# Optimization experiments

Hardware: AMD Instinct MI355X
Metric: run time of the kernel (lower is better)

The kernel has to match this reference:

```python
import jax, jax.numpy as jnp
import numpy as np

D_MODEL, DFF, OUT, SEQ = 256, 1024, 32, 512
SIGMA = 0.1          # sigma for q/k/v/z SMC noise
SIGMA_OBS = 0.5      # observation noise


def _layernorm(x, g, b, eps=1e-6):
    mu = jnp.mean(x, axis=-1, keepdims=True)
    var = jnp.mean(jnp.square(x - mu), axis=-1, keepdims=True)
    return (x - mu) * jax.lax.rsqrt(var + eps) * g + b


def _resample(params, i_t, t):
    # params: (B,P,S,D); i_t: (B,P) ancestor indices; resample only the past [:t+1]
    past = jnp.take_along_axis(params[:, :, :t + 1, :], i_t[:, :, None, None], axis=1)
    return jnp.concatenate([past, params[:, :, t + 1:, :]], axis=2)


def setup_inputs() -> dict:
    key = jax.random.key(0)
    ks = jax.random.split(key, 24)
    B, P = 32, 10
    d = {
        'x': jax.random.normal(ks[0], (B, P, D_MODEL), jnp.float32),
        'y': jax.random.normal(ks[1], (B, P, OUT), jnp.float32),
        'K': jax.random.normal(ks[2], (B, P, SEQ, D_MODEL), jnp.float32),
        'V': jax.random.normal(ks[3], (B, P, SEQ, D_MODEL), jnp.float32),
        'R': jax.random.normal(ks[4], (B, P, SEQ, D_MODEL), jnp.float32),
        'noise_q': jax.random.normal(ks[5], (B, P, 1, D_MODEL), jnp.float32),
        'noise_k': jax.random.normal(ks[6], (B, P, 1, D_MODEL), jnp.float32),
        'noise_v': jax.random.normal(ks[7], (B, P, 1, D_MODEL), jnp.float32),
        'noise_z': jax.random.normal(ks[8], (B, P, 1, D_MODEL), jnp.float32),
        'dec_timestep': 256,
    }
    s = 0.02
    d['wq_w'] = jax.random.normal(ks[9], (D_MODEL, D_MODEL), jnp.float32) * s
    d['wq_b'] = jnp.zeros((D_MODEL,), jnp.float32)
    d['wk_w'] = jax.random.normal(ks[10], (D_MODEL, D_MODEL), jnp.float32) * s
    d['wk_b'] = jnp.zeros((D_MODEL,), jnp.float32)
    d['wv_w'] = jax.random.normal(ks[11], (D_MODEL, D_MODEL), jnp.float32) * s
    d['wv_b'] = jnp.zeros((D_MODEL,), jnp.float32)
    d['wz_w'] = jax.random.normal(ks[12], (D_MODEL, D_MODEL), jnp.float32) * s
    d['wz_b'] = jnp.zeros((D_MODEL,), jnp.float32)
    d['ln1_g'] = jnp.ones((D_MODEL,), jnp.float32)
    d['ln1_b'] = jnp.zeros((D_MODEL,), jnp.float32)
    d['ffn_w1'] = jax.random.normal(ks[13], (D_MODEL, DFF), jnp.float32) * s
    d['ffn_b1'] = jnp.zeros((DFF,), jnp.float32)
    d['ffn_w2'] = jax.random.normal(ks[14], (DFF, D_MODEL), jnp.float32) * s
    d['ffn_b2'] = jnp.zeros((D_MODEL,), jnp.float32)
    d['ln2_g'] = jnp.ones((D_MODEL,), jnp.float32)
    d['ln2_b'] = jnp.zeros((D_MODEL,), jnp.float32)
    d['out_w'] = jax.random.normal(ks[15], (D_MODEL, OUT), jnp.float32) * s
    d['out_b'] = jnp.zeros((OUT,), jnp.float32)
    return d


def reference(x, y, K, V, R, noise_q, noise_k, noise_v, noise_z,
              wq_w, wq_b, wk_w, wk_b, wv_w, wv_b, wz_w, wz_b,
              ln1_g, ln1_b, ffn_w1, ffn_b1, ffn_w2, ffn_b2,
              ln2_g, ln2_b, out_w, out_b, dec_timestep):
    t = dec_timestep
    B, P, D = x.shape
    sq = jnp.sqrt(jnp.float32(SIGMA))
    xq = x[:, :, None, :]           # (B,P,1,D)
    yq = y[:, :, None, :]           # (B,P,1,F_y)
    # --- Self_Attention_SMC: project current token, add SMC gaussian noise ---
    q = xq @ wq_w + wq_b + sq * noise_q
    k = xq @ wk_w + wk_b + sq * noise_k
    v = xq @ wv_w + wv_b + sq * noise_v
    # in-place style KV cache update at timestep t (concat past/new/future)
    K = jnp.concatenate([K[:, :, :t, :], k, K[:, :, t + 1:, :]], axis=2)
    V = jnp.concatenate([V[:, :, :t, :], v, V[:, :, t + 1:, :]], axis=2)
    logits = jnp.einsum('bpod,bpsd->bpos', q, K) / jnp.sqrt(jnp.float32(D))
    attn_weights = jax.nn.softmax(logits, axis=-1)          # (B,P,1,S)
    z = jnp.einsum('bpos,bpsd->bpod', attn_weights, V)
    z = z @ wz_w + wz_b + sq * noise_z
    # --- full_model: layernorm + FFN + layernorm ---
    out = _layernorm(z + xq, ln1_g, ln1_b)
    r = jax.nn.relu(out @ ffn_w1 + ffn_b1) @ ffn_w2 + ffn_b2
    r = _layernorm(r + out, ln2_g, ln2_b)                   # (B,P,1,D)
    predictions = r @ out_w + out_b                          # (B,P,1,F_y)
    R = jnp.concatenate([R[:, :, :t, :], r, R[:, :, t + 1:, :]], axis=2)
    mu = jnp.squeeze(yq - predictions, axis=-2)              # (B,P,F_y)
    log_w = -jnp.sum(mu * mu, axis=-1) / (2.0 * SIGMA_OBS)   # (B,P)
    w = jax.nn.softmax(jnp.exp(log_w), axis=-1)              # faithful to original (softmax of exp)
    w = jax.lax.stop_gradient(w)
    # categorical resampling of ancestors (tf.random.categorical uses w as logits)
    i_t = jax.random.categorical(jax.random.key(42), w[:, None, :], shape=(B, P))
    i_t = jax.lax.stop_gradient(i_t)
    K = _resample(K, i_t, t)
    V = _resample(V, i_t, t)
    R = _resample(R, i_t, t)
    return r, attn_weights, K, V, R, w
```

## Files before the change

kernel.cpp:

```cpp
#include <hip/hip_runtime.h>
#include <hip/hip_bf16.h>
#include <stdint.h>

#define BATCH 32
#define NPART 10
#define BP_TOT 320
#define DM 256
#define FF 1024
#define OD 32
#define SL 512
#define NCHUNK 4
#define CROWS 128

#define SQRT_SIGMA 0.31622776601683794f

typedef float nfloat4 __attribute__((ext_vector_type(4)));

__device__ __forceinline__ void nt_store4(const float4& v, float* p) {
    nfloat4 nv;
    nv.x = v.x; nv.y = v.y; nv.z = v.z; nv.w = v.w;
    __builtin_nontemporal_store(nv, (nfloat4*)p);
}

__device__ __forceinline__ uint32_t rotl32(uint32_t x, uint32_t r) {
    return (x << r) | (x >> (32u - r));
}

__device__ __forceinline__ void threefry2x32(uint32_t k0, uint32_t k1,
                                             uint32_t x0, uint32_t x1,
                                             uint32_t& o0, uint32_t& o1) {
    uint32_t k2 = k0 ^ k1 ^ 0x1BD11BDAu;
    uint32_t x = x0 + k0, y = x1 + k1;
#define TFR(r) { x += y; y = rotl32(y, r); y ^= x; }
    TFR(13u) TFR(15u) TFR(26u) TFR(6u)
    x += k1; y += k2 + 1u;
    TFR(17u) TFR(29u) TFR(16u) TFR(24u)
    x += k2; y += k0 + 2u;
    TFR(13u) TFR(15u) TFR(26u) TFR(6u)
    x += k0; y += k1 + 3u;
    TFR(17u) TFR(29u) TFR(16u) TFR(24u)
    x += k1; y += k2 + 4u;
    TFR(13u) TFR(15u) TFR(26u) TFR(6u)
    x += k2; y += k0 + 5u;
#undef TFR
    o0 = x; o1 = y;
}

__device__ __forceinline__ float jax_gumbel_part(uint32_t m) {
    const float TINY = 1.17549435e-38f;
    uint32_t o0, o1;
    threefry2x32(0u, 42u, 0u, m, o0, o1);
    uint32_t bits = o0 ^ o1;
    uint32_t fb = (bits >> 9) | 0x3f800000u;
    float f = __uint_as_float(fb) - 1.0f;
    float u = fmaxf(TINY, f + TINY);
    return -logf(-logf(u));
}

__global__ __launch_bounds__(256) void qkv_kernel(
    const float* __restrict__ x,
    const float* __restrict__ nq, const float* __restrict__ nk,
    const float* __restrict__ nv,
    const float* __restrict__ wq_w, const float* __restrict__ wq_b,
    const float* __restrict__ wk_w, const float* __restrict__ wk_b,
    const float* __restrict__ wv_w, const float* __restrict__ wv_b,
    float* __restrict__ qtmp, float* __restrict__ knew, float* __restrict__ vnew)
{
    const int bb = blockIdx.x;
    const int m  = blockIdx.y;
    const int d  = threadIdx.x;

    __shared__ float xs[4][DM];
    #pragma unroll
    for (int g = 0; g < 4; ++g) xs[g][d] = x[(bb * 4 + g) * DM + d];
    __syncthreads();

    const float* W; const float* bias; const float* noise;
    if (m == 0)      { W = wq_w; bias = wq_b; noise = nq; }
    else if (m == 1) { W = wk_w; bias = wk_b; noise = nk; }
    else             { W = wv_w; bias = wv_b; noise = nv; }

    float a0 = 0.f, a1 = 0.f, a2 = 0.f, a3 = 0.f;
    #pragma unroll 4
    for (int i = 0; i < DM; ++i) {
        float wv = W[i * DM + d];
        a0 = fmaf(xs[0][i], wv, a0);
        a1 = fmaf(xs[1][i], wv, a1);
        a2 = fmaf(xs[2][i], wv, a2);
        a3 = fmaf(xs[3][i], wv, a3);
    }
    float r[4] = {a0, a1, a2, a3};
    #pragma unroll
    for (int g = 0; g < 4; ++g) {
        int bp = bb * 4 + g;
        float v = r[g] + bias[d] + SQRT_SIGMA * noise[bp * DM + d];
        if (m == 0)      qtmp[(size_t)bp * SL + d] = v;
        else if (m == 1) knew[(size_t)bp * DM + d] = v;
        else             vnew[(size_t)bp * DM + d] = v;
    }
}

__global__ __launch_bounds__(256) void attn_chunk_kernel(
    const float* __restrict__ Kin, const float* __restrict__ Vin,
    const float* __restrict__ knew, const float* __restrict__ vnew,
    const float* __restrict__ qtmp, const int* __restrict__ t_ptr,
    float* __restrict__ Kout, float* __restrict__ Vout,
    float* __restrict__ logits, float* __restrict__ zpart,
    float* __restrict__ mstat)
{
    const int bp   = blockIdx.x;
    const int sc   = blockIdx.y;
    const int tid  = threadIdx.x;
    const int lane = tid & 63;
    const int wave = tid >> 6;
    const int t    = *t_ptr;

    __shared__ float qs[DM], ks[DM], vs[DM];
    __shared__ float att_loc[CROWS];
    __shared__ float scratch[4 * 256];
    __shared__ float redm[2], rede[2];

    if (tid < DM) {
        qs[tid] = qtmp[(size_t)bp * SL + tid];
        ks[tid] = knew[(size_t)bp * DM + tid];
        vs[tid] = vnew[(size_t)bp * DM + tid];
    }
    __syncthreads();

    const float* Kbp = Kin + (size_t)bp * SL * DM;
    const float* Vbp = Vin + (size_t)bp * SL * DM;
    float4 q4 = *(const float4*)&qs[lane * 4];
    const int s0 = sc * CROWS + wave * 32;

    for (int j0 = 0; j0 < 32; j0 += 8) {
        float4 k4[8];
        #pragma unroll
        for (int u = 0; u < 8; ++u) {
            int s = s0 + j0 + u;
            k4[u] = (s == t) ? *(const float4*)&ks[lane * 4]
                             : *(const float4*)&Kbp[(size_t)s * DM + lane * 4];
        }
        #pragma unroll
        for (int u = 0; u < 8; ++u) {
            int s = s0 + j0 + u;
            if (s > t)
                nt_store4(k4[u], Kout + ((size_t)bp * SL + s) * DM + lane * 4);
            float acc = q4.x * k4[u].x + q4.y * k4[u].y + q4.z * k4[u].z + q4.w * k4[u].w;
            #pragma unroll
            for (int off = 32; off; off >>= 1) acc += __shfl_down(acc, off);
            if (lane == 0) {
                float l = acc * 0.0625f;
                att_loc[wave * 32 + j0 + u] = l;
                logits[(size_t)bp * SL + s] = l;
            }
        }
    }
    __syncthreads();

    float l = (tid < CROWS) ? att_loc[tid] : -3.402823466e+38f;
    float mm = l;
    #pragma unroll
    for (int off = 32; off; off >>= 1) mm = fmaxf(mm, __shfl_down(mm, off));
    if (tid < CROWS && lane == 0) redm[wave] = mm;
    __syncthreads();
    const float m_loc = fmaxf(redm[0], redm[1]);
    float p = (tid < CROWS) ? expf(l - m_loc) : 0.f;
    if (tid < CROWS) att_loc[tid] = p;
    float e = p;
    #pragma unroll
    for (int off = 32; off; off >>= 1) e += __shfl_down(e, off);
    if (tid < CROWS && lane == 0) rede[wave] = e;
    __syncthreads();
    const float e_loc = rede[0] + rede[1];

    float4 z4 = make_float4(0.f, 0.f, 0.f, 0.f);
    for (int j0 = 0; j0 < 32; j0 += 8) {
        float4 v4[8];
        #pragma unroll
        for (int u = 0; u < 8; ++u) {
            int s = s0 + j0 + u;
            v4[u] = (s == t) ? *(const float4*)&vs[lane * 4]
                             : *(const float4*)&Vbp[(size_t)s * DM + lane * 4];
        }
        #pragma unroll
        for (int u = 0; u < 8; ++u) {
            int s = s0 + j0 + u;
            if (s > t)
                nt_store4(v4[u], Vout + ((size_t)bp * SL + s) * DM + lane * 4);
            float a = att_loc[wave * 32 + j0 + u];
            z4.x = fmaf(a, v4[u].x, z4.x);
            z4.y = fmaf(a, v4[u].y, z4.y);
            z4.z = fmaf(a, v4[u].z, z4.z);
            z4.w = fmaf(a, v4[u].w, z4.w);
        }
    }
    *(float4*)&scratch[wave * 256 + lane * 4] = z4;
    __syncthreads();
    if (tid < DM) {
        float zp = (scratch[tid] + scratch[256 + tid]) + (scratch[512 + tid] + scratch[768 + tid]);
        zpart[((size_t)bp * NCHUNK + sc) * DM + tid] = zp;
    }
    if (tid == 0) {
        mstat[((size_t)bp * NCHUNK + sc) * 2 + 0] = m_loc;
        mstat[((size_t)bp * NCHUNK + sc) * 2 + 1] = e_loc;
    }
}

__global__ __launch_bounds__(1024) void post_kernel(
    const float* __restrict__ x, const float* __restrict__ nz,
    const float* __restrict__ logits, const float* __restrict__ zpart,
    const float* __restrict__ mstat,
    const float* __restrict__ wz_w, const float* __restrict__ wz_b,
    const float* __restrict__ ln1_g, const float* __restrict__ ln1_b,
    const float* __restrict__ w1, const float* __restrict__ b1,
    const float* __restrict__ w2, const float* __restrict__ b2,
    const float* __restrict__ ln2_g, const float* __restrict__ ln2_b,
    float* __restrict__ attn_out, float* __restrict__ r_out)
{
    const int bp   = blockIdx.x;
    const int tid  = threadIdx.x;
    const int lane = tid & 63;
    const int wave = tid >> 6;
    const int grp  = tid >> 8;
    const int qtid = tid & 255;

    __shared__ float buf[DM];
    __shared__ float xs[DM];
    __shared__ float hid[FF];
    __shared__ float scratch[1024];
    __shared__ float red[32];

    const float* ms = mstat + (size_t)bp * (2 * NCHUNK);
    float mc[NCHUNK], ec[NCHUNK];
    float gm = -3.402823466e+38f;
    #pragma unroll
    for (int c = 0; c < NCHUNK; ++c) {
        mc[c] = ms[2 * c]; ec[c] = ms[2 * c + 1];
        gm = fmaxf(gm, mc[c]);
    }
    float fc[NCHUNK], denom = 0.f;
    #pragma unroll
    for (int c = 0; c < NCHUNK; ++c) {
        fc[c] = expf(mc[c] - gm);
        denom = fmaf(ec[c], fc[c], denom);
    }
    const float inv = 1.0f / denom;

    if (tid < 512) {
        float l = logits[(size_t)bp * SL + tid];
        __builtin_nontemporal_store(expf(l - gm) * inv,
                                    attn_out + (size_t)bp * SL + tid);
    } else if (tid < 768) {
        int d = tid - 512;
        const float* zp = zpart + (size_t)bp * NCHUNK * DM;
        float z = 0.f;
        #pragma unroll
        for (int c = 0; c < NCHUNK; ++c) z = fmaf(zp[c * DM + d], fc[c], z);
        buf[d] = z * inv;
    } else {
        int d = tid - 768;
        xs[d] = x[bp * DM + d];
    }
    __syncthreads();

    {
        const int i0 = grp * 64;
        float a0 = 0.f, a1 = 0.f;
        #pragma unroll 4
        for (int ii = 0; ii < 32; ++ii) {
            a0 = fmaf(buf[i0 + ii],      wz_w[(i0 + ii)      * DM + qtid], a0);
            a1 = fmaf(buf[i0 + ii + 32], wz_w[(i0 + ii + 32) * DM + qtid], a1);
        }
        scratch[grp * 256 + qtid] = a0 + a1;
    }
    __syncthreads();
    float h = 0.f;
    if (tid < DM) {
        float az = (scratch[tid] + scratch[256 + tid]) + (scratch[512 + tid] + scratch[768 + tid]);
        h = az + wz_b[tid] + SQRT_SIGMA * nz[bp * DM + tid] + xs[tid];
    }

    float s1 = h;
    #pragma unroll
    for (int off = 32; off; off >>= 1) s1 += __shfl_down(s1, off);
    if (lane == 0) red[wave] = s1;
    __syncthreads();
    float mu = (red[0] + red[1] + red[2] + red[3]) * (1.0f / DM);
    float dv = (tid < DM) ? (h - mu) : 0.f;
    float s2 = dv * dv;
    #pragma unroll
    for (int off = 32; off; off >>= 1) s2 += __shfl_down(s2, off);
    if (lane == 0) red[16 + wave] = s2;
    __syncthreads();
    float var = (red[16] + red[17] + red[18] + red[19]) * (1.0f / DM);
    float o = 0.f;
    __syncthreads();
    if (tid < DM) {
        o = dv * rsqrtf(var + 1e-6f) * ln1_g[tid] + ln1_b[tid];
        buf[tid] = o;
    }
    __syncthreads();

    {
        float h0 = 0.f, h1 = 0.f, h2 = 0.f, h3 = 0.f;
        #pragma unroll 4
        for (int i = 0; i < 64; ++i) {
            h0 = fmaf(buf[i],       w1[(i      ) * FF + tid], h0);
            h1 = fmaf(buf[i +  64], w1[(i +  64) * FF + tid], h1);
            h2 = fmaf(buf[i + 128], w1[(i + 128) * FF + tid], h2);
            h3 = fmaf(buf[i + 192], w1[(i + 192) * FF + tid], h3);
        }
        hid[tid] = fmaxf((h0 + h1) + (h2 + h3) + b1[tid], 0.f);
    }
    __syncthreads();

    {
        const int i0 = grp * 256;
        float a0 = 0.f, a1 = 0.f, a2 = 0.f, a3 = 0.f;
        #pragma unroll 4
        for (int ii = 0; ii < 64; ++ii) {
            a0 = fmaf(hid[i0 + ii],       w2[(i0 + ii      ) * DM + qtid], a0);
            a1 = fmaf(hid[i0 + ii +  64], w2[(i0 + ii +  64) * DM + qtid], a1);
            a2 = fmaf(hid[i0 + ii + 128], w2[(i0 + ii + 128) * DM + qtid], a2);
            a3 = fmaf(hid[i0 + ii + 192], w2[(i0 + ii + 192) * DM + qtid], a3);
        }
        scratch[grp * 256 + qtid] = (a0 + a1) + (a2 + a3);
    }
    __syncthreads();
    float rr = 0.f;
    if (tid < DM) {
        rr = (scratch[tid] + scratch[256 + tid]) + (scratch[512 + tid] + scratch[768 + tid])
           + b2[tid] + o;
    }

    float t1 = rr;
    #pragma unroll
    for (int off = 32; off; off >>= 1) t1 += __shfl_down(t1, off);
    if (lane == 0) red[wave] = t1;
    __syncthreads();
    float mu2 = (red[0] + red[1] + red[2] + red[3]) * (1.0f / DM);
    float dv2 = (tid < DM) ? (rr - mu2) : 0.f;
    float t2 = dv2 * dv2;
    #pragma unroll
    for (int off = 32; off; off >>= 1) t2 += __shfl_down(t2, off);
    if (lane == 0) red[16 + wave] = t2;
    __syncthreads();
    float var2 = (red[16] + red[17] + red[18] + red[19]) * (1.0f / DM);
    if (tid < DM) {
        float rf = dv2 * rsqrtf(var2 + 1e-6f) * ln2_g[tid] + ln2_b[tid];
        r_out[(size_t)bp * DM + tid] = rf;
    }
}

__global__ __launch_bounds__(320) void weights_kernel(
    const float* __restrict__ r, const float* __restrict__ y,
    const float* __restrict__ out_w, const float* __restrict__ out_b,
    float* __restrict__ w_out, int* __restrict__ i_t)
{
    const int b   = blockIdx.x;
    const int tid = threadIdx.x;
    const int p   = tid >> 5;
    const int j   = tid & 31;

    __shared__ float sred[NPART];
    __shared__ float es[NPART];
    __shared__ float pe[NPART];
    __shared__ float wsm[NPART];

    const float* rrow = r + (size_t)(b * NPART + p) * DM;
    float acc = 0.f;
    #pragma unroll 4
    for (int i = 0; i < DM; ++i) acc = fmaf(rrow[i], out_w[i * OD + j], acc);
    float pred = acc + out_b[j];
    float muv  = y[(size_t)(b * NPART + p) * OD + j] - pred;
    float s    = muv * muv;
    #pragma unroll
    for (int off = 16; off; off >>= 1) s += __shfl_down(s, off, 32);
    if (j == 0) sred[p] = s;
    __syncthreads();

    if (tid < NPART) es[tid] = expf(-sred[tid]);
    __syncthreads();
    if (tid < NPART) {
        float mx = es[0];
        #pragma unroll
        for (int i = 1; i < NPART; ++i) mx = fmaxf(mx, es[i]);
        pe[tid] = expf(es[tid] - mx);
    }
    __syncthreads();
    if (tid < NPART) {
        float sum = 0.f;
        #pragma unroll
        for (int i = 0; i < NPART; ++i) sum += pe[i];
        float wv = pe[tid] / sum;
        w_out[b * NPART + tid] = wv;
        wsm[tid] = wv;
    }
    __syncthreads();

    if (tid < NPART) {
        int pp = tid;
        int best = 0;
        float bests = -3.402823466e+38f;
        #pragma unroll
        for (int jj = 0; jj < NPART; ++jj) {
            uint32_t m = (uint32_t)(b * 100 + pp * 10 + jj);
            float score = jax_gumbel_part(m) + wsm[jj];
            if (score > bests) { bests = score; best = jj; }
        }
        i_t[b * NPART + pp] = best;
    }
}

__global__ __launch_bounds__(256) void resample_kernel(
    const float* __restrict__ Kin, const float* __restrict__ Vin,
    const float* __restrict__ Rin,
    const float* __restrict__ knew, const float* __restrict__ vnew,
    const float* __restrict__ rnew,
    const int* __restrict__ i_t, const int* __restrict__ t_ptr,
    float* __restrict__ Kout, float* __restrict__ Vout, float* __restrict__ Rout)
{
    const int t    = *t_ptr;
    const int ysel = blockIdx.y;
    const int tid  = threadIdx.x;

    const float* gat = (ysel == 1) ? Kin : (ysel == 0) ? Vin : Rin;
    const float* nb  = (ysel == 1) ? knew : (ysel == 0) ? vnew : rnew;
    float* outb      = (ysel == 1) ? Kout : (ysel == 0) ? Vout : Rout;

    #pragma unroll
    for (int half = 0; half < 2; ++half) {
        size_t f4i = (size_t)blockIdx.x * 512 + half * 256 + tid;
        int lane4 = (int)(f4i & 63);
        int row   = (int)(f4i >> 6);
        int bpi   = row >> 9;
        int s     = row & 511;

        if (ysel != 2 && s > t) continue;

        int b     = bpi / NPART;
        int p     = bpi - b * NPART;
        int srcp  = (s <= t) ? i_t[bpi] : p;
        int src_bpi = b * NPART + srcp;

        const float* src = (s == t) ? nb + (size_t)src_bpi * DM
                                    : gat + ((size_t)src_bpi * SL + s) * DM;
        float4 v4 = *(const float4*)(src + (size_t)lane4 * 4);
        nt_store4(v4, outb + (size_t)row * DM + (size_t)lane4 * 4);
    }
}

extern "C" void kernel_launch(void* const* d_in, const int* in_sizes, int n_in,
                              void* d_out, int out_size, void* d_ws, size_t ws_size,
                              hipStream_t stream) {
    const float* x    = (const float*)d_in[0];
    const float* y    = (const float*)d_in[1];
    const float* Kin  = (const float*)d_in[2];
    const float* Vin  = (const float*)d_in[3];
    const float* Rin  = (const float*)d_in[4];
    const float* nq   = (const float*)d_in[5];
    const float* nk   = (const float*)d_in[6];
    const float* nv   = (const float*)d_in[7];
    const float* nz   = (const float*)d_in[8];
    const int*   tptr = (const int*)d_in[9];
    const float* wq_w = (const float*)d_in[10];
    const float* wq_b = (const float*)d_in[11];
    const float* wk_w = (const float*)d_in[12];
    const float* wk_b = (const float*)d_in[13];
    const float* wv_w = (const float*)d_in[14];
    const float* wv_b = (const float*)d_in[15];
    const float* wz_w = (const float*)d_in[16];
    const float* wz_b = (const float*)d_in[17];
    const float* ln1g = (const float*)d_in[18];
    const float* ln1b = (const float*)d_in[19];
    const float* w1   = (const float*)d_in[20];
    const float* b1   = (const float*)d_in[21];
    const float* w2   = (const float*)d_in[22];
    const float* b2   = (const float*)d_in[23];
    const float* ln2g = (const float*)d_in[24];
    const float* ln2b = (const float*)d_in[25];
    const float* outw = (const float*)d_in[26];
    const float* outb = (const float*)d_in[27];

    float* out = (float*)d_out;
    const size_t R_ELEMS    = (size_t)BP_TOT * DM;
    const size_t ATTN_ELEMS = (size_t)BP_TOT * SL;
    const size_t KVR_ELEMS  = (size_t)BP_TOT * SL * DM;
    float* r_out    = out;
    float* attn_out = out + R_ELEMS;
    float* K_out    = out + R_ELEMS + ATTN_ELEMS;
    float* V_out    = K_out + KVR_ELEMS;
    float* R_out    = V_out + KVR_ELEMS;
    float* w_out    = R_out + KVR_ELEMS;

    float* knew = (float*)d_ws;
    float* vnew = knew + R_ELEMS;
    int*   i_t  = (int*)(vnew + R_ELEMS);

    float* logits = R_out;
    float* zpart  = R_out + ATTN_ELEMS;
    float* mstat  = zpart + (size_t)BP_TOT * NCHUNK * DM;

    qkv_kernel<<<dim3(BP_TOT / 4, 3), 256, 0, stream>>>(
        x, nq, nk, nv, wq_w, wq_b, wk_w, wk_b, wv_w, wv_b,
        attn_out, knew, vnew);

    attn_chunk_kernel<<<dim3(BP_TOT, NCHUNK), 256, 0, stream>>>(
        Kin, Vin, knew, vnew, attn_out, tptr,
        K_out, V_out, logits, zpart, mstat);

    post_kernel<<<BP_TOT, 1024, 0, stream>>>(
        x, nz, logits, zpart, mstat,
        wz_w, wz_b, ln1g, ln1b, w1, b1, w2, b2, ln2g, ln2b,
        attn_out, r_out);

    weights_kernel<<<BATCH, 320, 0, stream>>>(
        r_out, y, outw, outb, w_out, i_t);

    resample_kernel<<<dim3(163840 / 8, 3), 256, 0, stream>>>(
        Kin, Vin, Rin, knew, vnew, r_out, i_t, tptr,
        K_out, V_out, R_out);
}
```

Measured before the change: 329.5 us.

## Fuse QKV projection into attention chunks and process two particles per post block

Removes the separate QKV kernel: each attention chunk block now computes q itself, and only the chunk containing timestep t computes the new k and v rows, which it also writes out for the resample step. The post kernel now handles two particles per block so every weight load (wz, w1, w2) is reused twice, halving weight traffic. In exchange q is recomputed redundantly across the four chunks, the has_t chunk does extra work that delays it, and the post kernel runs only 160 blocks.

```diff
diff --git a/kernel.cpp b/kernel.cpp
--- a/kernel.cpp
+++ b/kernel.cpp
@@ -57,53 +57,16 @@
     return -logf(-logf(u));
 }
 
-__global__ __launch_bounds__(256) void qkv_kernel(
+__global__ __launch_bounds__(256) void attn_chunk_kernel(
+    const float* __restrict__ Kin, const float* __restrict__ Vin,
     const float* __restrict__ x,
     const float* __restrict__ nq, const float* __restrict__ nk,
     const float* __restrict__ nv,
     const float* __restrict__ wq_w, const float* __restrict__ wq_b,
     const float* __restrict__ wk_w, const float* __restrict__ wk_b,
     const float* __restrict__ wv_w, const float* __restrict__ wv_b,
-    float* __restrict__ qtmp, float* __restrict__ knew, float* __restrict__ vnew)
-{
-    const int bb = blockIdx.x;
-    const int m  = blockIdx.y;
-    const int d  = threadIdx.x;
-
-    __shared__ float xs[4][DM];
-    #pragma unroll
-    for (int g = 0; g < 4; ++g) xs[g][d] = x[(bb * 4 + g) * DM + d];
-    __syncthreads();
-
-    const float* W; const float* bias; const float* noise;
-    if (m == 0)      { W = wq_w; bias = wq_b; noise = nq; }
-    else if (m == 1) { W = wk_w; bias = wk_b; noise = nk; }
-    else             { W = wv_w; bias = wv_b; noise = nv; }
-
-    float a0 = 0.f, a1 = 0.f, a2 = 0.f, a3 = 0.f;
-    #pragma unroll 4
-    for (int i = 0; i < DM; ++i) {
-        float wv = W[i * DM + d];
-        a0 = fmaf(xs[0][i], wv, a0);
-        a1 = fmaf(xs[1][i], wv, a1);
-        a2 = fmaf(xs[2][i], wv, a2);
-        a3 = fmaf(xs[3][i], wv, a3);
-    }
-    float r[4] = {a0, a1, a2, a3};
-    #pragma unroll
-    for (int g = 0; g < 4; ++g) {
-        int bp = bb * 4 + g;
-        float v = r[g] + bias[d] + SQRT_SIGMA * noise[bp * DM + d];
-        if (m == 0)      qtmp[(size_t)bp * SL + d] = v;
-        else if (m == 1) knew[(size_t)bp * DM + d] = v;
-        else             vnew[(size_t)bp * DM + d] = v;
-    }
-}
-
-__global__ __launch_bounds__(256) void attn_chunk_kernel(
-    const float* __restrict__ Kin, const float* __restrict__ Vin,
-    const float* __restrict__ knew, const float* __restrict__ vnew,
-    const float* __restrict__ qtmp, const int* __restrict__ t_ptr,
+    const int* __restrict__ t_ptr,
+    float* __restrict__ knew, float* __restrict__ vnew,
     float* __restrict__ Kout, float* __restrict__ Vout,
     float* __restrict__ logits, float* __restrict__ zpart,
     float* __restrict__ mstat)
@@ -115,22 +78,56 @@
     const int wave = tid >> 6;
     const int t    = *t_ptr;
 
-    __shared__ float qs[DM], ks[DM], vs[DM];
+    __shared__ float xs[DM], qs[DM], ks[DM], vs[DM];
     __shared__ float att_loc[CROWS];
     __shared__ float scratch[4 * 256];
     __shared__ float redm[2], rede[2];
 
-    if (tid < DM) {
-        qs[tid] = qtmp[(size_t)bp * SL + tid];
-        ks[tid] = knew[(size_t)bp * DM + tid];
-        vs[tid] = vnew[(size_t)bp * DM + tid];
+    xs[tid] = x[bp * DM + tid];
+    __syncthreads();
+
+    {
+        float a0 = 0.f, a1 = 0.f, a2 = 0.f, a3 = 0.f;
+        #pragma unroll 4
+        for (int i = 0; i < 64; ++i) {
+            a0 = fmaf(xs[i],       wq_w[(i      ) * DM + tid], a0);
+            a1 = fmaf(xs[i +  64], wq_w[(i +  64) * DM + tid], a1);
+            a2 = fmaf(xs[i + 128], wq_w[(i + 128) * DM + tid], a2);
+            a3 = fmaf(xs[i + 192], wq_w[(i + 192) * DM + tid], a3);
+        }
+        qs[tid] = (a0 + a1) + (a2 + a3) + wq_b[tid]
+                + SQRT_SIGMA * nq[bp * DM + tid];
+    }
+
+    const int s0c = sc * CROWS;
+    const bool has_t = (t >= s0c) && (t < s0c + CROWS);
+    if (has_t) {
+        float k0 = 0.f, k1 = 0.f, k2 = 0.f, k3 = 0.f;
+        float v0 = 0.f, v1 = 0.f, v2 = 0.f, v3 = 0.f;
+        #pragma unroll 2
+        for (int i = 0; i < 64; ++i) {
+            float x0 = xs[i], x1 = xs[i + 64], x2 = xs[i + 128], x3 = xs[i + 192];
+            k0 = fmaf(x0, wk_w[(i      ) * DM + tid], k0);
+            k1 = fmaf(x1, wk_w[(i +  64) * DM + tid], k1);
+            k2 = fmaf(x2, wk_w[(i + 128) * DM + tid], k2);
+            k3 = fmaf(x3, wk_w[(i + 192) * DM + tid], k3);
+            v0 = fmaf(x0, wv_w[(i      ) * DM + tid], v0);
+            v1 = fmaf(x1, wv_w[(i +  64) * DM + tid], v1);
+            v2 = fmaf(x2, wv_w[(i + 128) * DM + tid], v2);
+            v3 = fmaf(x3, wv_w[(i + 192) * DM + tid], v3);
+        }
+        float kv = (k0 + k1) + (k2 + k3) + wk_b[tid] + SQRT_SIGMA * nk[bp * DM + tid];
+        float vv = (v0 + v1) + (v2 + v3) + wv_b[tid] + SQRT_SIGMA * nv[bp * DM + tid];
+        ks[tid] = kv; vs[tid] = vv;
+        knew[(size_t)bp * DM + tid] = kv;
+        vnew[(size_t)bp * DM + tid] = vv;
     }
     __syncthreads();
 
     const float* Kbp = Kin + (size_t)bp * SL * DM;
     const float* Vbp = Vin + (size_t)bp * SL * DM;
     float4 q4 = *(const float4*)&qs[lane * 4];
-    const int s0 = sc * CROWS + wave * 32;
+    const int s0 = s0c + wave * 32;
 
     for (int j0 = 0; j0 < 32; j0 += 8) {
         float4 k4[8];
@@ -217,138 +214,152 @@
     const float* __restrict__ ln2_g, const float* __restrict__ ln2_b,
     float* __restrict__ attn_out, float* __restrict__ r_out)
 {
-    const int bp   = blockIdx.x;
+    const int bb   = blockIdx.x;
     const int tid  = threadIdx.x;
     const int lane = tid & 63;
-    const int wave = tid >> 6;
-    const int grp  = tid >> 8;
-    const int qtid = tid & 255;
-
-    __shared__ float buf[DM];
-    __shared__ float xs[DM];
-    __shared__ float hid[FF];
-    __shared__ float scratch[1024];
-    __shared__ float red[32];
-
-    const float* ms = mstat + (size_t)bp * (2 * NCHUNK);
-    float mc[NCHUNK], ec[NCHUNK];
-    float gm = -3.402823466e+38f;
-    #pragma unroll
-    for (int c = 0; c < NCHUNK; ++c) {
-        mc[c] = ms[2 * c]; ec[c] = ms[2 * c + 1];
-        gm = fmaxf(gm, mc[c]);
-    }
-    float fc[NCHUNK], denom = 0.f;
-    #pragma unroll
-    for (int c = 0; c < NCHUNK; ++c) {
-        fc[c] = expf(mc[c] - gm);
-        denom = fmaf(ec[c], fc[c], denom);
-    }
-    const float inv = 1.0f / denom;
-
-    if (tid < 512) {
-        float l = logits[(size_t)bp * SL + tid];
-        __builtin_nontemporal_store(expf(l - gm) * inv,
-                                    attn_out + (size_t)bp * SL + tid);
-    } else if (tid < 768) {
-        int d = tid - 512;
-        const float* zp = zpart + (size_t)bp * NCHUNK * DM;
+    const int bp0  = bb * 2;
+
+    __shared__ float bufz[2][DM];
+    __shared__ float xs2[2][DM];
+    __shared__ float hid[2][FF];
+    __shared__ float part[4][2][DM];
+    __shared__ float red[2][8];
+
+    float gmv[2], invv[2], fcs[2][NCHUNK];
+    #pragma unroll
+    for (int g = 0; g < 2; ++g) {
+        const float* ms = mstat + (size_t)(bp0 + g) * (2 * NCHUNK);
+        float mc[NCHUNK], ec[NCHUNK];
+        float gm = -3.402823466e+38f;
+        #pragma unroll
+        for (int c = 0; c < NCHUNK; ++c) {
+            mc[c] = ms[2 * c]; ec[c] = ms[2 * c + 1];
+            gm = fmaxf(gm, mc[c]);
+        }
+        float denom = 0.f;
+        #pragma unroll
+        for (int c = 0; c < NCHUNK; ++c) {
+            fcs[g][c] = expf(mc[c] - gm);
+            denom = fmaf(ec[c], fcs[g][c], denom);
+        }
+        gmv[g] = gm; invv[g] = 1.0f / denom;
+    }
+
+    {
+        int ga = tid >> 9, s = tid & 511;
+        float l = logits[(size_t)(bp0 + ga) * SL + s];
+        __builtin_nontemporal_store(expf(l - gmv[ga]) * invv[ga],
+                                    attn_out + (size_t)(bp0 + ga) * SL + s);
+    }
+    if (tid < 512) {
+        int g = tid >> 8, d = tid & 255;
+        const float* zp = zpart + (size_t)(bp0 + g) * NCHUNK * DM;
         float z = 0.f;
         #pragma unroll
-        for (int c = 0; c < NCHUNK; ++c) z = fmaf(zp[c * DM + d], fc[c], z);
-        buf[d] = z * inv;
+        for (int c = 0; c < NCHUNK; ++c) z = fmaf(zp[c * DM + d], fcs[g][c], z);
+        bufz[g][d] = z * invv[g];
     } else {
-        int d = tid - 768;
-        xs[d] = x[bp * DM + d];
+        int r2 = tid - 512;
+        int g = r2 >> 8, d = r2 & 255;
+        xs2[g][d] = x[(size_t)(bp0 + g) * DM + d];
     }
     __syncthreads();
 
     {
-        const int i0 = grp * 64;
-        float a0 = 0.f, a1 = 0.f;
-        #pragma unroll 4
-        for (int ii = 0; ii < 32; ++ii) {
-            a0 = fmaf(buf[i0 + ii],      wz_w[(i0 + ii)      * DM + qtid], a0);
-            a1 = fmaf(buf[i0 + ii + 32], wz_w[(i0 + ii + 32) * DM + qtid], a1);
-        }
-        scratch[grp * 256 + qtid] = a0 + a1;
-    }
-    __syncthreads();
-    float h = 0.f;
-    if (tid < DM) {
-        float az = (scratch[tid] + scratch[256 + tid]) + (scratch[512 + tid] + scratch[768 + tid]);
-        h = az + wz_b[tid] + SQRT_SIGMA * nz[bp * DM + tid] + xs[tid];
-    }
-
-    float s1 = h;
-    #pragma unroll
-    for (int off = 32; off; off >>= 1) s1 += __shfl_down(s1, off);
-    if (lane == 0) red[wave] = s1;
-    __syncthreads();
-    float mu = (red[0] + red[1] + red[2] + red[3]) * (1.0f / DM);
-    float dv = (tid < DM) ? (h - mu) : 0.f;
-    float s2 = dv * dv;
-    #pragma unroll
-    for (int off = 32; off; off >>= 1) s2 += __shfl_down(s2, off);
-    if (lane == 0) red[16 + wave] = s2;
-    __syncthreads();
-    float var = (red[16] + red[17] + red[18] + red[19]) * (1.0f / DM);
-    float o = 0.f;
-    __syncthreads();
-    if (tid < DM) {
-        o = dv * rsqrtf(var + 1e-6f) * ln1_g[tid] + ln1_b[tid];
-        buf[tid] = o;
-    }
-    __syncthreads();
-
-    {
-        float h0 = 0.f, h1 = 0.f, h2 = 0.f, h3 = 0.f;
-        #pragma unroll 4
-        for (int i = 0; i < 64; ++i) {
-            h0 = fmaf(buf[i],       w1[(i      ) * FF + tid], h0);
-            h1 = fmaf(buf[i +  64], w1[(i +  64) * FF + tid], h1);
-            h2 = fmaf(buf[i + 128], w1[(i + 128) * FF + tid], h2);
-            h3 = fmaf(buf[i + 192], w1[(i + 192) * FF + tid], h3);
-        }
-        hid[tid] = fmaxf((h0 + h1) + (h2 + h3) + b1[tid], 0.f);
-    }
-    __syncthreads();
-
-    {
-        const int i0 = grp * 256;
-        float a0 = 0.f, a1 = 0.f, a2 = 0.f, a3 = 0.f;
+        int ic = tid >> 8, d = tid & 255;
+        const int i0 = ic * 64;
+        float p0 = 0.f, p1 = 0.f;
         #pragma unroll 4
         for (int ii = 0; ii < 64; ++ii) {
-            a0 = fmaf(hid[i0 + ii],       w2[(i0 + ii      ) * DM + qtid], a0);
-            a1 = fmaf(hid[i0 + ii +  64], w2[(i0 + ii +  64) * DM + qtid], a1);
-            a2 = fmaf(hid[i0 + ii + 128], w2[(i0 + ii + 128) * DM + qtid], a2);
-            a3 = fmaf(hid[i0 + ii + 192], w2[(i0 + ii + 192) * DM + qtid], a3);
-        }
-        scratch[grp * 256 + qtid] = (a0 + a1) + (a2 + a3);
+            float wv = wz_w[(i0 + ii) * DM + d];
+            p0 = fmaf(bufz[0][i0 + ii], wv, p0);
+            p1 = fmaf(bufz[1][i0 + ii], wv, p1);
+        }
+        part[ic][0][d] = p0; part[ic][1][d] = p1;
+    }
+    __syncthreads();
+
+    const int gg = (tid >> 8) & 1;
+    const int dd = tid & 255;
+    const int wv4 = (tid >> 6) & 3;
+    float h = 0.f, o = 0.f;
+    if (tid < 512) {
+        float az = (part[0][gg][dd] + part[1][gg][dd]) + (part[2][gg][dd] + part[3][gg][dd]);
+        h = az + wz_b[dd] + SQRT_SIGMA * nz[(size_t)(bp0 + gg) * DM + dd] + xs2[gg][dd];
+    }
+
+    float s1 = h;
+    #pragma unroll
+    for (int off = 32; off; off >>= 1) s1 += __shfl_down(s1, off);
+    if (tid < 512 && lane == 0) red[gg][wv4] = s1;
+    __syncthreads();
+    if (tid < 512) {
+        float mu = (red[gg][0] + red[gg][1] + red[gg][2] + red[gg][3]) * (1.0f / DM);
+        h -= mu;
+    }
+    float s2 = h * h;
+    #pragma unroll
+    for (int off = 32; off; off >>= 1) s2 += __shfl_down(s2, off);
+    if (tid < 512 && lane == 0) red[gg][4 + wv4] = s2;
+    __syncthreads();
+    if (tid < 512) {
+        float var = (red[gg][4] + red[gg][5] + red[gg][6] + red[gg][7]) * (1.0f / DM);
+        o = h * rsqrtf(var + 1e-6f) * ln1_g[dd] + ln1_b[dd];
+        bufz[gg][dd] = o;
+    }
+    __syncthreads();
+
+    {
+        float c0 = 0.f, c1 = 0.f;
+        #pragma unroll 4
+        for (int i = 0; i < DM; ++i) {
+            float wv = w1[i * FF + tid];
+            c0 = fmaf(bufz[0][i], wv, c0);
+            c1 = fmaf(bufz[1][i], wv, c1);
+        }
+        float bb1 = b1[tid];
+        hid[0][tid] = fmaxf(c0 + bb1, 0.f);
+        hid[1][tid] = fmaxf(c1 + bb1, 0.f);
+    }
+    __syncthreads();
+
+    {
+        int ic = tid >> 8, d = tid & 255;
+        const int i0 = ic * 256;
+        float p0 = 0.f, p1 = 0.f;
+        #pragma unroll 4
+        for (int ii = 0; ii < 256; ++ii) {
+            float wv = w2[(i0 + ii) * DM + d];
+            p0 = fmaf(hid[0][i0 + ii], wv, p0);
+            p1 = fmaf(hid[1][i0 + ii], wv, p1);
+        }
+        part[ic][0][d] = p0; part[ic][1][d] = p1;
     }
     __syncthreads();
     float rr = 0.f;
-    if (tid < DM) {
-        rr = (scratch[tid] + scratch[256 + tid]) + (scratch[512 + tid] + scratch[768 + tid])
-           + b2[tid] + o;
+    if (tid < 512) {
+        rr = (part[0][gg][dd] + part[1][gg][dd]) + (part[2][gg][dd] + part[3][gg][dd])
+           + b2[dd] + o;
     }
 
     float t1 = rr;
     #pragma unroll
     for (int off = 32; off; off >>= 1) t1 += __shfl_down(t1, off);
-    if (lane == 0) red[wave] = t1;
-    __syncthreads();
-    float mu2 = (red[0] + red[1] + red[2] + red[3]) * (1.0f / DM);
-    float dv2 = (tid < DM) ? (rr - mu2) : 0.f;
-    float t2 = dv2 * dv2;
+    if (tid < 512 && lane == 0) red[gg][wv4] = t1;
+    __syncthreads();
+    if (tid < 512) {
+        float mu2 = (red[gg][0] + red[gg][1] + red[gg][2] + red[gg][3]) * (1.0f / DM);
+        rr -= mu2;
+    }
+    float t2 = rr * rr;
     #pragma unroll
     for (int off = 32; off; off >>= 1) t2 += __shfl_down(t2, off);
-    if (lane == 0) red[16 + wave] = t2;
-    __syncthreads();
-    float var2 = (red[16] + red[17] + red[18] + red[19]) * (1.0f / DM);
-    if (tid < DM) {
-        float rf = dv2 * rsqrtf(var2 + 1e-6f) * ln2_g[tid] + ln2_b[tid];
-        r_out[(size_t)bp * DM + tid] = rf;
+    if (tid < 512 && lane == 0) red[gg][4 + wv4] = t2;
+    __syncthreads();
+    if (tid < 512) {
+        float var2 = (red[gg][4] + red[gg][5] + red[gg][6] + red[gg][7]) * (1.0f / DM);
+        float rf = rr * rsqrtf(var2 + 1e-6f) * ln2_g[dd] + ln2_b[dd];
+        r_out[(size_t)(bp0 + gg) * DM + dd] = rf;
     }
 }
 
@@ -501,15 +512,12 @@
     float* zpart  = R_out + ATTN_ELEMS;
     float* mstat  = zpart + (size_t)BP_TOT * NCHUNK * DM;
 
-    qkv_kernel<<<dim3(BP_TOT / 4, 3), 256, 0, stream>>>(
-        x, nq, nk, nv, wq_w, wq_b, wk_w, wk_b, wv_w, wv_b,
-        attn_out, knew, vnew);
-
     attn_chunk_kernel<<<dim3(BP_TOT, NCHUNK), 256, 0, stream>>>(
-        Kin, Vin, knew, vnew, attn_out, tptr,
-        K_out, V_out, logits, zpart, mstat);
-
-    post_kernel<<<BP_TOT, 1024, 0, stream>>>(
+        Kin, Vin, x, nq, nk, nv,
+        wq_w, wq_b, wk_w, wk_b, wv_w, wv_b, tptr,
+        knew, vnew, K_out, V_out, logits, zpart, mstat);
+
+    post_kernel<<<BP_TOT / 2, 1024, 0, stream>>>(
         x, nz, logits, zpart, mstat,
         wz_w, wz_b, ln1g, ln1b, w1, b1, w2, b2, ln2g, ln2b,
         attn_out, r_out);
```

Result: slower. 342.4 us (+3.9%).
